# Optimization experiments

Hardware: AMD Instinct MI355X
Metric: run time of the kernel (lower is better)

Reference implementation:

```python
import jax, jax.numpy as jnp
import numpy as np

EMBED = 1024
HEADS = 16
HEAD_DIM = EMBED // HEADS


def setup_inputs() -> dict:
    key = jax.random.key(0)
    ks = jax.random.split(key, 6)
    scale = 1.0 / np.sqrt(EMBED)
    x = jax.random.normal(ks[0], (2, 2048, EMBED), dtype=jnp.float32)
    # nn.Linear weights stored as [out_features, in_features]
    Wq = jax.random.normal(ks[1], (EMBED, EMBED), dtype=jnp.float32) * scale
    Wk = jax.random.normal(ks[2], (EMBED, EMBED), dtype=jnp.float32) * scale
    Wv = jax.random.normal(ks[3], (EMBED, EMBED), dtype=jnp.float32) * scale
    Wo = jax.random.normal(ks[4], (EMBED, EMBED), dtype=jnp.float32) * scale
    bo = jax.random.normal(ks[5], (EMBED,), dtype=jnp.float32) * scale
    return {"x": x, "Wq": Wq, "Wk": Wk, "Wv": Wv, "Wo": Wo, "bo": bo}


def reference(x, Wq, Wk, Wv, Wo, bo):
    N, L, E = x.shape
    # projections (torch Linear: x @ W.T)
    q = (x @ Wq.T).reshape(N, L, HEADS, HEAD_DIM).transpose(0, 2, 1, 3)  # [N,H,L,D]
    k = (x @ Wk.T).reshape(N, L, HEADS, HEAD_DIM).transpose(0, 2, 1, 3)
    v = (x @ Wv.T).reshape(N, L, HEADS, HEAD_DIM).transpose(0, 2, 1, 3)
    # scores scaled by sqrt(embed_size) (as in source, not sqrt(head_dim))
    scores = jnp.einsum("nhqd,nhkd->nhqk", q, k) / jnp.sqrt(jnp.float32(E))
    attn = jax.nn.softmax(scores, axis=-1)
    out = jnp.einsum("nhqk,nhkd->nhqd", attn, v)  # [N,H,L,D]
    out = out.transpose(0, 2, 1, 3).reshape(N, L, E)
    return out @ Wo.T + bo
```

## Files before the change

### kernel.cpp

```cpp
#include <hip/hip_runtime.h>
#include <hip/hip_bf16.h>

constexpr int NB  = 2;
constexpr int SL  = 2048;
constexpr int EMB = 1024;
constexpr int NH  = 16;
constexpr int HD  = 64;
constexpr int MT  = NB * SL;
constexpr size_t PROJ = (size_t)MT * EMB;

typedef __attribute__((ext_vector_type(8))) short bf16x8;
typedef __attribute__((ext_vector_type(4))) float f32x4;

__device__ inline short f2b(float f) {
  __hip_bfloat16 b = __float2bfloat16(f);
  short s; __builtin_memcpy(&s, &b, 2); return s;
}

#define GLDS16(g, l)                                                     \
  __builtin_amdgcn_global_load_lds(                                      \
      (const __attribute__((address_space(1))) void*)(g),                \
      (__attribute__((address_space(3))) void*)(l), 16, 0, 0)

__global__ __launch_bounds__(256) void cast_all(
    const float* __restrict__ x,  const float* __restrict__ wq,
    const float* __restrict__ wk, const float* __restrict__ wv,
    const float* __restrict__ wo, short* __restrict__ xb,
    short* __restrict__ wqkv, short* __restrict__ wob) {
  const size_t t = (size_t)blockIdx.x * 256 + threadIdx.x;
  const float* src; short* dst; size_t base;
  if (t < 1048576)      { src = x;  dst = xb;              base = 0; }
  else if (t < 1310720) { src = wq; dst = wqkv;            base = 1048576; }
  else if (t < 1572864) { src = wk; dst = wqkv + (1 << 20); base = 1310720; }
  else if (t < 1835008) { src = wv; dst = wqkv + (2 << 20); base = 1572864; }
  else                  { src = wo; dst = wob;             base = 1835008; }
  const size_t i = t - base;
  const float4 v = ((const float4*)src)[i];
  const short4 o = {f2b(v.x), f2b(v.y), f2b(v.z), f2b(v.w)};
  ((short4*)dst)[i] = o;
}

__global__ __launch_bounds__(256) void gemm_qkv(
    const short* __restrict__ A, const short* __restrict__ W,
    short* __restrict__ qb, short* __restrict__ kb, short* __restrict__ vt) {
  __shared__ short As[128 * 32];
  __shared__ short Bs[128 * 32];
  const int tid = threadIdx.x;
  const int w = tid >> 6, lane = tid & 63;
  const int la = lane >> 4, lb = lane & 15;
  const int wm = w & 1, wn = w >> 1;
  const int m0 = blockIdx.y << 7, n0 = blockIdx.x << 7;
  const int srow = lane >> 2, scol = (lane & 3) << 3;
  const short* a0 = A + (size_t)(m0 + w * 16 + srow) * 1024 + scol;
  const short* b0 = W + (size_t)(n0 + w * 16 + srow) * 1024 + scol;
  short* lA0 = As + (w * 16) * 32;
  short* lA1 = As + (64 + w * 16) * 32;
  short* lB0 = Bs + (w * 16) * 32;
  short* lB1 = Bs + (64 + w * 16) * 32;

  f32x4 acc[4][4];
#pragma unroll
  for (int i = 0; i < 4; ++i)
#pragma unroll
    for (int j = 0; j < 4; ++j) acc[i][j] = (f32x4){0.f, 0.f, 0.f, 0.f};

  for (int k0 = 0; k0 < 1024; k0 += 32) {
    __syncthreads();
    GLDS16(a0 + k0, lA0);
    GLDS16(a0 + 64 * 1024 + k0, lA1);
    GLDS16(b0 + k0, lB0);
    GLDS16(b0 + 64 * 1024 + k0, lB1);
    __syncthreads();
    bf16x8 af[4], bf[4];
#pragma unroll
    for (int i = 0; i < 4; ++i)
      af[i] = *(const bf16x8*)&As[(wm * 64 + i * 16 + lb) * 32 + la * 8];
#pragma unroll
    for (int j = 0; j < 4; ++j)
      bf[j] = *(const bf16x8*)&Bs[(wn * 64 + j * 16 + lb) * 32 + la * 8];
#pragma unroll
    for (int i = 0; i < 4; ++i)
#pragma unroll
      for (int j = 0; j < 4; ++j)
        acc[i][j] = __builtin_amdgcn_mfma_f32_16x16x32_bf16(af[i], bf[j],
                                                            acc[i][j], 0, 0, 0);
  }

  const int region = n0 >> 10;
  if (region < 2) {
    short* dst = region ? kb : qb;
    const float sc = region ? 1.0f : 0.03125f * 1.44269504f;
    const int nb0 = n0 & 1023;
#pragma unroll
    for (int j = 0; j < 4; ++j) {
      const int nj = nb0 + wn * 64 + j * 16 + lb;
#pragma unroll
      for (int i = 0; i < 4; ++i) {
        const int mi = m0 + wm * 64 + i * 16 + la * 4;
#pragma unroll
        for (int r = 0; r < 4; ++r)
          dst[(size_t)(mi + r) * 1024 + nj] = f2b(acc[i][j][r] * sc);
      }
    }
  } else {
#pragma unroll
    for (int j = 0; j < 4; ++j) {
      const int nv = (n0 - 2048) + wn * 64 + j * 16 + lb;
      const int h = nv >> 6, d = nv & 63;
#pragma unroll
      for (int i = 0; i < 4; ++i) {
        const int mi = m0 + wm * 64 + i * 16 + la * 4;
        const int nbi = mi >> 11, seq = mi & (SL - 1);
        const int k5 = seq & 31;
        const int seqp = (seq & ~31) | (8 * ((k5 >> 2) & 3) + 4 * (k5 >> 4));
        const short4 o = {f2b(acc[i][j][0]), f2b(acc[i][j][1]),
                          f2b(acc[i][j][2]), f2b(acc[i][j][3])};
        *(short4*)&vt[((size_t)(nbi * NH + h) * HD + d) * SL + seqp] = o;
      }
    }
  }
}

__global__ __launch_bounds__(256) void gemm_out(
    const short* __restrict__ A, const short* __restrict__ W,
    const float* __restrict__ bias, float* __restrict__ out) {
  __shared__ short As[128 * 32];
  __shared__ short Bs[64 * 32];
  const int tid = threadIdx.x;
  const int w = tid >> 6, lane = tid & 63;
  const int la = lane >> 4, lb = lane & 15;
  const int wm = w & 1, wn = w >> 1;
  const int m0 = blockIdx.y << 7, n0 = blockIdx.x << 6;
  const int srow = lane >> 2, scol = (lane & 3) << 3;
  const short* a0 = A + (size_t)(m0 + w * 16 + srow) * 1024 + scol;
  const short* b0 = W + (size_t)(n0 + w * 16 + srow) * 1024 + scol;
  short* lA0 = As + (w * 16) * 32;
  short* lA1 = As + (64 + w * 16) * 32;
  short* lB0 = Bs + (w * 16) * 32;

  f32x4 acc[4][2];
#pragma unroll
  for (int i = 0; i < 4; ++i)
#pragma unroll
    for (int j = 0; j < 2; ++j) acc[i][j] = (f32x4){0.f, 0.f, 0.f, 0.f};

  for (int k0 = 0; k0 < 1024; k0 += 32) {
    __syncthreads();
    GLDS16(a0 + k0, lA0);
    GLDS16(a0 + 64 * 1024 + k0, lA1);
    GLDS16(b0 + k0, lB0);
    __syncthreads();
    bf16x8 af[4], bf[2];
#pragma unroll
    for (int i = 0; i < 4; ++i)
      af[i] = *(const bf16x8*)&As[(wm * 64 + i * 16 + lb) * 32 + la * 8];
#pragma unroll
    for (int j = 0; j < 2; ++j)
      bf[j] = *(const bf16x8*)&Bs[(wn * 32 + j * 16 + lb) * 32 + la * 8];
#pragma unroll
    for (int i = 0; i < 4; ++i)
#pragma unroll
      for (int j = 0; j < 2; ++j)
        acc[i][j] = __builtin_amdgcn_mfma_f32_16x16x32_bf16(af[i], bf[j],
                                                            acc[i][j], 0, 0, 0);
  }
#pragma unroll
  for (int j = 0; j < 2; ++j) {
    const int nj = n0 + wn * 32 + j * 16 + lb;
    const float bv = bias[nj];
#pragma unroll
    for (int i = 0; i < 4; ++i) {
      const int mi = m0 + wm * 64 + i * 16 + la * 4;
#pragma unroll
      for (int r = 0; r < 4; ++r)
        out[(size_t)(mi + r) * 1024 + nj] = acc[i][j][r] + bv;
    }
  }
}

__global__ __launch_bounds__(256, 2) void attn_mfma(const short* __restrict__ Qg,
                                                    const short* __restrict__ Kg,
                                                    const short* __restrict__ Vtg,
                                                    short* __restrict__ Ab) {
  __shared__ __align__(16) char smem[34816];
  __shared__ float lred[128];
  short (*Ks)[72] = (short(*)[72])smem;
  short (*Vt)[72] = (short(*)[72])(smem + 64 * 72 * 2);
  float* red = (float*)smem;
  const int tid = threadIdx.x;
  const int w = tid >> 6, lane = tid & 63;
  const int G = lane >> 4, lb = lane & 15;
  const int wk = w & 1, wq = w >> 1;
  const int qt = blockIdx.x, h = blockIdx.y, n = blockIdx.z;
  const int row = tid >> 3, c = (tid & 7) << 3;

  const short* Qb = Qg + ((size_t)(n * SL + (qt << 7) + 64 * wq)) * EMB + h * HD;
  bf16x8 bQ[4][2];
#pragma unroll
  for (int nt = 0; nt < 4; ++nt)
#pragma unroll
    for (int ks = 0; ks < 2; ++ks)
      bQ[nt][ks] =
          *(const bf16x8*)(Qb + (size_t)(16 * nt + lb) * EMB + 32 * ks + 8 * G);

  f32x4 O[4][4];
  float lacc[4] = {0.f, 0.f, 0.f, 0.f};
#pragma unroll
  for (int i = 0; i < 4; ++i)
#pragma unroll
    for (int j = 0; j < 4; ++j) O[i][j] = (f32x4){0.f, 0.f, 0.f, 0.f};

  const short* Kb0 = Kg + ((size_t)(n * SL)) * EMB + h * HD;
  const short* Vb0 = Vtg + ((size_t)(n * NH + h)) * HD * SL;

  bf16x8 pk[2], pv[2];
#pragma unroll
  for (int k = 0; k < 2; ++k) {
    pk[k] = *(const bf16x8*)(Kb0 + (size_t)(row + 32 * k) * EMB + c);
    pv[k] = *(const bf16x8*)(Vb0 + (size_t)(row + 32 * k) * SL + c);
  }

  for (int kt = 0; kt < SL / 64; ++kt) {
    __syncthreads();
#pragma unroll
    for (int k = 0; k < 2; ++k) {
      *(bf16x8*)&Ks[row + 32 * k][c] = pk[k];
      *(bf16x8*)&Vt[row + 32 * k][c] = pv[k];
    }
    __syncthreads();
    if (kt + 1 < SL / 64) {
      const short* Kb = Kb0 + (size_t)(kt + 1) * 64 * EMB;
      const short* Vb = Vb0 + (size_t)(kt + 1) * 64;
#pragma unroll
      for (int k = 0; k < 2; ++k) {
        pk[k] = *(const bf16x8*)(Kb + (size_t)(row + 32 * k) * EMB + c);
        pv[k] = *(const bf16x8*)(Vb + (size_t)(row + 32 * k) * SL + c);
      }
    }

    f32x4 S[2][4];
#pragma unroll
    for (int mt = 0; mt < 2; ++mt)
#pragma unroll
      for (int nt = 0; nt < 4; ++nt) S[mt][nt] = (f32x4){0.f, 0.f, 0.f, 0.f};
#pragma unroll
    for (int ks = 0; ks < 2; ++ks) {
      const bf16x8 aK0 = *(const bf16x8*)&Ks[32 * wk + lb][32 * ks + 8 * G];
      const bf16x8 aK1 = *(const bf16x8*)&Ks[32 * wk + 16 + lb][32 * ks + 8 * G];
#pragma unroll
      for (int nt = 0; nt < 4; ++nt) {
        S[0][nt] = __builtin_amdgcn_mfma_f32_16x16x32_bf16(aK0, bQ[nt][ks],
                                                           S[0][nt], 0, 0, 0);
        S[1][nt] = __builtin_amdgcn_mfma_f32_16x16x32_bf16(aK1, bQ[nt][ks],
                                                           S[1][nt], 0, 0, 0);
      }
    }

#pragma unroll
    for (int nt = 0; nt < 4; ++nt)
#pragma unroll
      for (int mt = 0; mt < 2; ++mt)
#pragma unroll
        for (int r = 0; r < 4; ++r) {
          const float p = __builtin_amdgcn_exp2f(S[mt][nt][r]);
          S[mt][nt][r] = p;
          lacc[nt] += p;
        }

    bf16x8 aV[4];
#pragma unroll
    for (int mtd = 0; mtd < 4; ++mtd)
      aV[mtd] = *(const bf16x8*)&Vt[16 * mtd + lb][32 * wk + 8 * G];
#pragma unroll
    for (int nt = 0; nt < 4; ++nt) {
      bf16x8 B2;
      B2[0] = f2b(S[0][nt][0]);
      B2[1] = f2b(S[0][nt][1]);
      B2[2] = f2b(S[0][nt][2]);
      B2[3] = f2b(S[0][nt][3]);
      B2[4] = f2b(S[1][nt][0]);
      B2[5] = f2b(S[1][nt][1]);
      B2[6] = f2b(S[1][nt][2]);
      B2[7] = f2b(S[1][nt][3]);
#pragma unroll
      for (int mtd = 0; mtd < 4; ++mtd)
        O[mtd][nt] = __builtin_amdgcn_mfma_f32_16x16x32_bf16(aV[mtd], B2,
                                                             O[mtd][nt], 0, 0, 0);
    }
  }

#pragma unroll
  for (int nt = 0; nt < 4; ++nt) {
    lacc[nt] += __shfl_xor(lacc[nt], 16);
    lacc[nt] += __shfl_xor(lacc[nt], 32);
  }

  __syncthreads();
  if (wk == 1) {
#pragma unroll
    for (int nt = 0; nt < 4; ++nt) {
      const int q = 16 * nt + lb;
#pragma unroll
      for (int mtd = 0; mtd < 4; ++mtd)
        *(f32x4*)&red[wq * 4352 + q * 68 + 16 * mtd + 4 * G] = O[mtd][nt];
      if (G == 0) lred[wq * 64 + q] = lacc[nt];
    }
  }
  __syncthreads();
  if (wk == 0) {
    short* Ao = Ab + ((size_t)(n * SL + (qt << 7) + 64 * wq)) * EMB + h * HD;
#pragma unroll
    for (int nt = 0; nt < 4; ++nt) {
      const int q = 16 * nt + lb;
      const float inv = 1.f / (lacc[nt] + lred[wq * 64 + q]);
#pragma unroll
      for (int mtd = 0; mtd < 4; ++mtd) {
        const f32x4 t = *(const f32x4*)&red[wq * 4352 + q * 68 + 16 * mtd + 4 * G];
        const f32x4 s = t + O[mtd][nt];
        const short4 o = {f2b(s[0] * inv), f2b(s[1] * inv), f2b(s[2] * inv),
                          f2b(s[3] * inv)};
        *(short4*)(Ao + (size_t)q * EMB + 16 * mtd + 4 * G) = o;
      }
    }
  }
}

extern "C" void kernel_launch(void* const* d_in, const int* in_sizes, int n_in,
                              void* d_out, int out_size, void* d_ws, size_t ws_size,
                              hipStream_t stream) {
  const float* x  = (const float*)d_in[0];
  const float* Wq = (const float*)d_in[1];
  const float* Wk = (const float*)d_in[2];
  const float* Wv = (const float*)d_in[3];
  const float* Wo = (const float*)d_in[4];
  const float* bo = (const float*)d_in[5];
  float* out = (float*)d_out;

  short* xb   = (short*)d_ws;
  short* wqkv = xb + PROJ;
  short* wob  = wqkv + 3u * EMB * EMB;
  short* qb   = wob + (size_t)EMB * EMB;
  short* kb   = qb + PROJ;
  short* vt   = kb + PROJ;
  short* ab   = qb;

  cast_all<<<8192, 256, 0, stream>>>(x, Wq, Wk, Wv, Wo, xb, wqkv, wob);
  gemm_qkv<<<dim3(24, 32), 256, 0, stream>>>(xb, wqkv, qb, kb, vt);
  attn_mfma<<<dim3(SL / 128, NH, NB), 256, 0, stream>>>(qb, kb, vt, ab);
  gemm_out<<<dim3(16, 32), 256, 0, stream>>>(ab, wob, bo, out);
}
```

Before: 178.9 us.

## Double-buffer 128-key K/V tiles in attention and reorder grid head-major

The attention kernel now stages 128-key tiles of K and V^T into two alternating shared-memory buffers, so each loop iteration needs one barrier instead of two and handles twice as many keys. Each wave processes two 32-key sub-tiles per iteration. The grid is reordered so consecutive blocks cover different heads of the same query tile, which changes how K/V are reused through L2. Shared memory per block grows to about 70KB, which may reduce occupancy below the two blocks per CU the launch bounds ask for, and more prefetch registers are held live.

```diff
diff --git a/kernel.cpp b/kernel.cpp
--- a/kernel.cpp
+++ b/kernel.cpp
@@ -182,17 +182,15 @@
                                                     const short* __restrict__ Kg,
                                                     const short* __restrict__ Vtg,
                                                     short* __restrict__ Ab) {
-  __shared__ __align__(16) char smem[34816];
+  __shared__ __align__(16) short smem[2 * 17920];
   __shared__ float lred[128];
-  short (*Ks)[72] = (short(*)[72])smem;
-  short (*Vt)[72] = (short(*)[72])(smem + 64 * 72 * 2);
-  float* red = (float*)smem;
   const int tid = threadIdx.x;
   const int w = tid >> 6, lane = tid & 63;
   const int G = lane >> 4, lb = lane & 15;
   const int wk = w & 1, wq = w >> 1;
-  const int qt = blockIdx.x, h = blockIdx.y, n = blockIdx.z;
-  const int row = tid >> 3, c = (tid & 7) << 3;
+  const int h = blockIdx.x, qt = blockIdx.y, n = blockIdx.z;
+  const int krow = tid >> 3, kcol = (tid & 7) << 3;
+  const int vrow = tid >> 4, vcol = (tid & 15) << 3;
 
   const short* Qb = Qg + ((size_t)(n * SL + (qt << 7) + 64 * wq)) * EMB + h * HD;
   bf16x8 bQ[4][2];
@@ -213,79 +211,89 @@
   const short* Kb0 = Kg + ((size_t)(n * SL)) * EMB + h * HD;
   const short* Vb0 = Vtg + ((size_t)(n * NH + h)) * HD * SL;
 
-  bf16x8 pk[2], pv[2];
-#pragma unroll
-  for (int k = 0; k < 2; ++k) {
-    pk[k] = *(const bf16x8*)(Kb0 + (size_t)(row + 32 * k) * EMB + c);
-    pv[k] = *(const bf16x8*)(Vb0 + (size_t)(row + 32 * k) * SL + c);
-  }
-
-  for (int kt = 0; kt < SL / 64; ++kt) {
-    __syncthreads();
-#pragma unroll
-    for (int k = 0; k < 2; ++k) {
-      *(bf16x8*)&Ks[row + 32 * k][c] = pk[k];
-      *(bf16x8*)&Vt[row + 32 * k][c] = pv[k];
-    }
-    __syncthreads();
-    if (kt + 1 < SL / 64) {
-      const short* Kb = Kb0 + (size_t)(kt + 1) * 64 * EMB;
-      const short* Vb = Vb0 + (size_t)(kt + 1) * 64;
-#pragma unroll
-      for (int k = 0; k < 2; ++k) {
-        pk[k] = *(const bf16x8*)(Kb + (size_t)(row + 32 * k) * EMB + c);
-        pv[k] = *(const bf16x8*)(Vb + (size_t)(row + 32 * k) * SL + c);
-      }
-    }
-
-    f32x4 S[2][4];
-#pragma unroll
-    for (int mt = 0; mt < 2; ++mt)
-#pragma unroll
-      for (int nt = 0; nt < 4; ++nt) S[mt][nt] = (f32x4){0.f, 0.f, 0.f, 0.f};
-#pragma unroll
-    for (int ks = 0; ks < 2; ++ks) {
-      const bf16x8 aK0 = *(const bf16x8*)&Ks[32 * wk + lb][32 * ks + 8 * G];
-      const bf16x8 aK1 = *(const bf16x8*)&Ks[32 * wk + 16 + lb][32 * ks + 8 * G];
+  bf16x8 pk[4], pv[4];
+#pragma unroll
+  for (int k = 0; k < 4; ++k)
+    pk[k] = *(const bf16x8*)(Kb0 + (size_t)(krow + 32 * k) * EMB + kcol);
+#pragma unroll
+  for (int r = 0; r < 4; ++r)
+    pv[r] = *(const bf16x8*)(Vb0 + (size_t)(vrow + 16 * r) * SL + vcol);
+
+  for (int kt = 0; kt < SL / 128; ++kt) {
+    short* Ks = &smem[(kt & 1) * 17920];
+    short* Vt = Ks + 128 * 72;
+#pragma unroll
+    for (int k = 0; k < 4; ++k)
+      *(bf16x8*)&Ks[(krow + 32 * k) * 72 + kcol] = pk[k];
+#pragma unroll
+    for (int r = 0; r < 4; ++r)
+      *(bf16x8*)&Vt[(vrow + 16 * r) * 136 + vcol] = pv[r];
+    __syncthreads();
+
+    if (kt + 1 < SL / 128) {
+      const short* Kb = Kb0 + (size_t)(kt + 1) * 128 * EMB;
+#pragma unroll
+      for (int k = 0; k < 4; ++k)
+        pk[k] = *(const bf16x8*)(Kb + (size_t)(krow + 32 * k) * EMB + kcol);
+#pragma unroll
+      for (int r = 0; r < 4; ++r)
+        pv[r] = *(const bf16x8*)(Vb0 + (size_t)(vrow + 16 * r) * SL +
+                                 (kt + 1) * 128 + vcol);
+    }
+
+#pragma unroll
+    for (int s = 0; s < 2; ++s) {
+      const int kb = 64 * wk + 32 * s;
+      f32x4 S[2][4];
+#pragma unroll
+      for (int mt = 0; mt < 2; ++mt)
+#pragma unroll
+        for (int nt = 0; nt < 4; ++nt) S[mt][nt] = (f32x4){0.f, 0.f, 0.f, 0.f};
+#pragma unroll
+      for (int ks = 0; ks < 2; ++ks) {
+        const bf16x8 aK0 = *(const bf16x8*)&Ks[(kb + lb) * 72 + 32 * ks + 8 * G];
+        const bf16x8 aK1 =
+            *(const bf16x8*)&Ks[(kb + 16 + lb) * 72 + 32 * ks + 8 * G];
+#pragma unroll
+        for (int nt = 0; nt < 4; ++nt) {
+          S[0][nt] = __builtin_amdgcn_mfma_f32_16x16x32_bf16(aK0, bQ[nt][ks],
+                                                             S[0][nt], 0, 0, 0);
+          S[1][nt] = __builtin_amdgcn_mfma_f32_16x16x32_bf16(aK1, bQ[nt][ks],
+                                                             S[1][nt], 0, 0, 0);
+        }
+      }
+
+#pragma unroll
+      for (int nt = 0; nt < 4; ++nt)
+#pragma unroll
+        for (int mt = 0; mt < 2; ++mt)
+#pragma unroll
+          for (int r = 0; r < 4; ++r) {
+            const float p = __builtin_amdgcn_exp2f(S[mt][nt][r]);
+            S[mt][nt][r] = p;
+            lacc[nt] += p;
+          }
+
+      bf16x8 aV[4];
+#pragma unroll
+      for (int mtd = 0; mtd < 4; ++mtd)
+        aV[mtd] = *(const bf16x8*)&Vt[(16 * mtd + lb) * 136 + kb + 8 * G];
 #pragma unroll
       for (int nt = 0; nt < 4; ++nt) {
-        S[0][nt] = __builtin_amdgcn_mfma_f32_16x16x32_bf16(aK0, bQ[nt][ks],
-                                                           S[0][nt], 0, 0, 0);
-        S[1][nt] = __builtin_amdgcn_mfma_f32_16x16x32_bf16(aK1, bQ[nt][ks],
-                                                           S[1][nt], 0, 0, 0);
-      }
-    }
-
-#pragma unroll
-    for (int nt = 0; nt < 4; ++nt)
-#pragma unroll
-      for (int mt = 0; mt < 2; ++mt)
-#pragma unroll
-        for (int r = 0; r < 4; ++r) {
-          const float p = __builtin_amdgcn_exp2f(S[mt][nt][r]);
-          S[mt][nt][r] = p;
-          lacc[nt] += p;
-        }
-
-    bf16x8 aV[4];
-#pragma unroll
-    for (int mtd = 0; mtd < 4; ++mtd)
-      aV[mtd] = *(const bf16x8*)&Vt[16 * mtd + lb][32 * wk + 8 * G];
-#pragma unroll
-    for (int nt = 0; nt < 4; ++nt) {
-      bf16x8 B2;
-      B2[0] = f2b(S[0][nt][0]);
-      B2[1] = f2b(S[0][nt][1]);
-      B2[2] = f2b(S[0][nt][2]);
-      B2[3] = f2b(S[0][nt][3]);
-      B2[4] = f2b(S[1][nt][0]);
-      B2[5] = f2b(S[1][nt][1]);
-      B2[6] = f2b(S[1][nt][2]);
-      B2[7] = f2b(S[1][nt][3]);
-#pragma unroll
-      for (int mtd = 0; mtd < 4; ++mtd)
-        O[mtd][nt] = __builtin_amdgcn_mfma_f32_16x16x32_bf16(aV[mtd], B2,
-                                                             O[mtd][nt], 0, 0, 0);
+        bf16x8 B2;
+        B2[0] = f2b(S[0][nt][0]);
+        B2[1] = f2b(S[0][nt][1]);
+        B2[2] = f2b(S[0][nt][2]);
+        B2[3] = f2b(S[0][nt][3]);
+        B2[4] = f2b(S[1][nt][0]);
+        B2[5] = f2b(S[1][nt][1]);
+        B2[6] = f2b(S[1][nt][2]);
+        B2[7] = f2b(S[1][nt][3]);
+#pragma unroll
+        for (int mtd = 0; mtd < 4; ++mtd)
+          O[mtd][nt] = __builtin_amdgcn_mfma_f32_16x16x32_bf16(aV[mtd], B2,
+                                                               O[mtd][nt], 0, 0, 0);
+      }
     }
   }
 
@@ -295,6 +303,7 @@
     lacc[nt] += __shfl_xor(lacc[nt], 32);
   }
 
+  float* red = (float*)smem;
   __syncthreads();
   if (wk == 1) {
 #pragma unroll
@@ -346,6 +355,6 @@
 
   cast_all<<<8192, 256, 0, stream>>>(x, Wq, Wk, Wv, Wo, xb, wqkv, wob);
   gemm_qkv<<<dim3(24, 32), 256, 0, stream>>>(xb, wqkv, qb, kb, vt);
-  attn_mfma<<<dim3(SL / 128, NH, NB), 256, 0, stream>>>(qb, kb, vt, ab);
+  attn_mfma<<<dim3(NH, SL / 128, NB), 256, 0, stream>>>(qb, kb, vt, ab);
   gemm_out<<<dim3(16, 32), 256, 0, stream>>>(ab, wob, bo, out);
 }
```

Result: no change. 178.8 us (-0.1%).
